# Performance work log

Hardware: AMD Instinct MI355X
Metric: run time of the kernel (lower is better)

The kernel has to match this reference:

```python
import jax, jax.numpy as jnp
import numpy as np

SCORE_THRESHOLD = 0.3
IOU_THRESHOLD = 0.5
TOP_K = 200
MAX_NMS_SIZE = 100
NEG = jnp.float32(-1e30)
NEG_HALF = jnp.float32(-1e29)


def _nms_per_class(scores, boxes):
    """Exact greedy NMS for one class. scores [N], boxes [N,4] (y1,x1,y2,x2).
    Returns (sel_scores [M], sel_boxes [M,4], valids [M]) with M=MAX_NMS_SIZE,
    zero-padded where fewer than M boxes survive (matches tf pad behavior)."""
    N = scores.shape[0]
    areas = jnp.prod(boxes[:, 2:] - boxes[:, :2], axis=-1)  # [N]
    arange_n = jnp.arange(N)
    # tf.image.non_max_suppression drops boxes with score < score_threshold
    masked0 = jnp.where(scores > SCORE_THRESHOLD, scores, NEG)

    def step(masked, _):
        idx = jnp.argmax(masked)
        s = masked[idx]
        valid = s > NEG_HALF
        box = boxes[idx]
        # IoU of selected box vs all boxes
        yx1 = jnp.maximum(box[:2], boxes[:, :2])
        yx2 = jnp.minimum(box[2:], boxes[:, 2:])
        inter = jnp.prod(jnp.maximum(yx2 - yx1, 0.0), axis=-1)
        union = jnp.prod(box[2:] - box[:2]) + areas - inter
        iou = jnp.where(union > 0, inter / union, 0.0)
        suppress = (iou > IOU_THRESHOLD) | (arange_n == idx)
        masked = jnp.where(valid & suppress, NEG, masked)
        return masked, (idx, valid, jnp.where(valid, s, 0.0))

    _, (idxs, valids, sel_scores) = jax.lax.scan(step, masked0, None, length=MAX_NMS_SIZE)
    sel_boxes = jnp.where(valids[:, None], boxes[idxs], 0.0)
    return sel_scores, sel_boxes, valids


def _per_sample(scores, boxes):
    """scores [N,C], boxes [N,4] -> (top_k_scores [K,2], top_k_boxes [K,4])."""
    cls_scores = scores[:, 1:].T  # [C-1, N]; class 0 (background) skipped
    sel_scores, sel_boxes, valids = jax.vmap(_nms_per_class, in_axes=(0, None))(cls_scores, boxes)
    ncls = cls_scores.shape[0]
    class_ids = jnp.where(valids, jnp.arange(1, ncls + 1, dtype=jnp.float32)[:, None], 0.0)
    flat_scores = jnp.stack([class_ids, sel_scores], axis=-1).reshape(-1, 2)  # [(C-1)*M, 2]
    flat_boxes = sel_boxes.reshape(-1, 4)
    n = flat_scores.shape[0]
    if TOP_K > n:  # static shapes -> Python-level pad branch
        flat_scores = jnp.pad(flat_scores, ((0, TOP_K - n), (0, 0)))
        flat_boxes = jnp.pad(flat_boxes, ((0, TOP_K - n), (0, 0)))
    _, top_idx = jax.lax.top_k(flat_scores[:, 1], TOP_K)
    return flat_scores[top_idx], flat_boxes[top_idx]


def setup_inputs() -> dict:
    key = jax.random.key(0)
    k1, k2, k3 = jax.random.split(key, 3)
    B, N, C = 16, 16384, 91
    scores_pred = jax.random.uniform(k1, (B, N, C), dtype=jnp.float32)
    tl = jax.random.uniform(k2, (B, N, 2), dtype=jnp.float32) * 0.8
    wh = jax.random.uniform(k3, (B, N, 2), dtype=jnp.float32) * 0.2 + 0.01
    boxes_pred = jnp.concatenate([tl, tl + wh], axis=-1)  # valid corner boxes
    return {"scores_pred": scores_pred, "boxes_pred": boxes_pred}


@jax.jit
def reference(scores_pred, boxes_pred):
    return jax.vmap(_per_sample)(scores_pred, boxes_pred)
```

## Files before the change

kernel.cpp:

```cpp
#include <hip/hip_runtime.h>

#define NTH 256
#define NBOX 16384
#define NCLSIN 91
#define NCLS 90
#define MAXSEL 100
#define TOPK 200
#define TSEL 256
#define CAP 1024
#define CANDL 512
#define CBCAP 256
#define BINS 1024
#define GRP 4
#define T0 0.989f
#define BOXPB 256
#define KSL 16
#define OVFC 64
#define CNTSTR 16

__device__ __forceinline__ unsigned fmap(float f) {
    unsigned u = __float_as_uint(f);
    return (u & 0x80000000u) ? ~u : (u | 0x80000000u);
}
__device__ __forceinline__ float funmap(unsigned u) {
    unsigned b = (u & 0x80000000u) ? (u ^ 0x80000000u) : ~u;
    return __uint_as_float(b);
}
__device__ __forceinline__ unsigned long long shfl_xor_u64(unsigned long long v, int mask) {
    unsigned lo = (unsigned)(v & 0xFFFFFFFFull);
    unsigned hi = (unsigned)(v >> 32);
    lo = __shfl_xor(lo, mask, 64);
    hi = __shfl_xor(hi, mask, 64);
    return ((unsigned long long)hi << 32) | (unsigned long long)lo;
}

__device__ __forceinline__ bool sup_test(float4 s, float sa, float4 c, float ca) {
    float y1 = fmaxf(s.x, c.x);
    float x1 = fmaxf(s.y, c.y);
    float y2 = fminf(s.z, c.z);
    float x2 = fminf(s.w, c.w);
    float dy = fmaxf(__fsub_rn(y2, y1), 0.f);
    float dx = fmaxf(__fsub_rn(x2, x1), 0.f);
    float inter = __fmul_rn(dy, dx);
    float uni = __fsub_rn(__fadd_rn(sa, ca), inter);
    if (!(uni > 0.f)) return false;
    float t = 0.5f * uni;
    if (inter <= t) return false;
    if (inter > __fmul_rn(t, 1.0000005f)) return true;
    return __fdiv_rn(inter, uni) > 0.5f;
}
__device__ __forceinline__ float box_area(float4 b) {
    return __fmul_rn(__fsub_rn(b.z, b.x), __fsub_rn(b.w, b.y));
}

__global__ __launch_bounds__(NTH) void zero_k(int4* __restrict__ p, int n4) {
    int i = blockIdx.x * NTH + threadIdx.x;
    if (i < n4) p[i] = make_int4(0, 0, 0, 0);
}

__device__ __forceinline__ void bin_select(unsigned* hist, unsigned* gbuf,
                                           int* sh_g, int* sh_b, unsigned* sh_pb,
                                           int tid, unsigned need) {
    unsigned gs = 0;
#pragma unroll
    for (int q = 0; q < GRP; ++q) gs += hist[tid * GRP + q];
    gbuf[tid] = gs;
    __syncthreads();
    for (int off = 1; off < NTH; off <<= 1) {
        unsigned add = (tid >= off) ? gbuf[tid - off] : 0u;
        __syncthreads();
        gbuf[tid] += add;
        __syncthreads();
    }
    if (tid == 0) *sh_g = NTH - 1;
    __syncthreads();
    if (gbuf[tid] >= need && (tid == 0 || gbuf[tid - 1] < need)) *sh_g = tid;
    __syncthreads();
    if (tid == 0) {
        int g = *sh_g;
        unsigned acc = (g > 0) ? gbuf[g - 1] : 0u;
        int bs = g * GRP + (GRP - 1);
        unsigned pb = acc;
#pragma unroll
        for (int q = 0; q < GRP; ++q) {
            acc += hist[g * GRP + q];
            if (acc >= need) { bs = g * GRP + q; pb = acc; break; }
            pb = acc;
        }
        *sh_b = bs; *sh_pb = pb;
    }
    __syncthreads();
}

__device__ __forceinline__ void sort_desc(unsigned long long* cand, int M, int tid) {
    int P = 1;
    while (P < M) P <<= 1;
    for (int i = M + tid; i < P; i += NTH) cand[i] = 0ull;
    __syncthreads();
    for (int kk = 2; kk <= P; kk <<= 1) {
        for (int jj = kk >> 1; jj > 0; jj >>= 1) {
            for (int i = tid; i < P; i += NTH) {
                int ixj = i ^ jj;
                if (ixj > i) {
                    unsigned long long a = cand[i], c = cand[ixj];
                    bool sw = ((i & kk) == 0) ? (a < c) : (a > c);
                    if (sw) { cand[i] = c; cand[ixj] = a; }
                }
            }
            __syncthreads();
        }
    }
}

__device__ __forceinline__ void emit_hit(unsigned long long pk, int b, int n0,
                                         int* cnt_s, unsigned long long* ent,
                                         unsigned* ovf_meta,
                                         unsigned long long* ovf_key,
                                         int* sh_ovf, int* cnt_g) {
    unsigned ee = (unsigned)pk;
    int row = (int)ee / NCLSIN;
    int c = (int)ee - row * NCLSIN;
    if (c == 0) return;
    unsigned i = (unsigned)(n0 + row);
    unsigned long long key = (pk & 0xFFFFFFFF00000000ull) | (0xFFFFFFFFu - i);
    int r = atomicAdd(&cnt_s[c], 1);
    if (r < KSL) {
        ent[c * KSL + r] = key;
    } else {
        int o = atomicAdd(sh_ovf, 1);
        if (o < OVFC) {
            ovf_meta[o] = ((unsigned)c << 16) | (unsigned)r;
            ovf_key[o] = key;
        } else {
            atomicAdd(&cnt_g[(b * NCLS + c - 1) * CNTSTR], CAP + 1);
        }
    }
}

__global__ __launch_bounds__(NTH) void filter_k(const float* __restrict__ in,
                                                unsigned long long* __restrict__ cand_g,
                                                int* __restrict__ cnt_g) {
    __shared__ int cnt_s[NCLSIN];
    __shared__ int base_s[NCLSIN];
    __shared__ unsigned long long ent[NCLSIN * KSL];
    __shared__ unsigned ovf_meta[OVFC];
    __shared__ unsigned long long ovf_key[OVFC];
    __shared__ int sh_ovf;

    const int tid = threadIdx.x;
    const int n0 = blockIdx.x * BOXPB;
    const int b = blockIdx.y;
    const int NF4 = BOXPB * NCLSIN / 4;

    for (int i = tid; i < NCLSIN; i += NTH) cnt_s[i] = 0;
    if (tid == 0) sh_ovf = 0;
    __syncthreads();

    unsigned long long q0 = 0, q1 = 0, q2 = 0, q3 = 0;
    int lc = 0;

    const float4* src = (const float4*)(in + ((size_t)b * NBOX + n0) * NCLSIN);
    for (int i = tid; i < NF4; i += 2 * NTH) {
        float4 v1 = src[i];
        int i2 = i + NTH;
        bool has2 = i2 < NF4;
        float4 v2 = make_float4(0.f, 0.f, 0.f, 0.f);
        if (has2) v2 = src[i2];
        float mx1 = fmaxf(fmaxf(v1.x, v1.y), fmaxf(v1.z, v1.w));
        float mx2 = fmaxf(fmaxf(v2.x, v2.y), fmaxf(v2.z, v2.w));
        if (fmaxf(mx1, mx2) > T0) {
#pragma unroll
            for (int h = 0; h < 2; ++h) {
                float4 v = h ? v2 : v1;
                float mx = h ? mx2 : mx1;
                int eb = (h ? i2 : i) * 4;
                if (mx > T0) {
                    const float sv[4] = {v.x, v.y, v.z, v.w};
#pragma unroll
                    for (int qq = 0; qq < 4; ++qq) {
                        float s = sv[qq];
                        if (s > T0) {
                            unsigned long long pk =
                                ((unsigned long long)fmap(s) << 32) |
                                (unsigned)(eb + qq);
                            if (lc == 0) q0 = pk;
                            else if (lc == 1) q1 = pk;
                            else if (lc == 2) q2 = pk;
                            else if (lc == 3) q3 = pk;
                            else emit_hit(pk, b, n0, cnt_s, ent, ovf_meta,
                                          ovf_key, &sh_ovf, cnt_g);
                            ++lc;
                        }
                    }
                }
            }
        }
    }
    if (lc > 0) emit_hit(q0, b, n0, cnt_s, ent, ovf_meta, ovf_key, &sh_ovf, cnt_g);
    if (lc > 1) emit_hit(q1, b, n0, cnt_s, ent, ovf_meta, ovf_key, &sh_ovf, cnt_g);
    if (lc > 2) emit_hit(q2, b, n0, cnt_s, ent, ovf_meta, ovf_key, &sh_ovf, cnt_g);
    if (lc > 3) emit_hit(q3, b, n0, cnt_s, ent, ovf_meta, ovf_key, &sh_ovf, cnt_g);
    __syncthreads();

    if (tid >= 1 && tid < NCLSIN) {
        int c = tid;
        int n = cnt_s[c];
        int base = 0;
        if (n > 0) {
            int bc = b * NCLS + c - 1;
            base = atomicAdd(&cnt_g[bc * CNTSTR], n);
            int lim = n < KSL ? n : KSL;
            for (int j = 0; j < lim; ++j) {
                int pos = base + j;
                if (pos < CAP) cand_g[(size_t)bc * CAP + pos] = ent[c * KSL + j];
            }
        }
        base_s[c] = base;
    }
    __syncthreads();

    int no = sh_ovf < OVFC ? sh_ovf : OVFC;
    for (int o = tid; o < no; o += NTH) {
        unsigned m = ovf_meta[o];
        int c = (int)(m >> 16);
        int r = (int)(m & 0xFFFFu);
        int bc = b * NCLS + c - 1;
        int pos = base_s[c] + r;
        if (pos < CAP) cand_g[(size_t)bc * CAP + pos] = ovf_key[o];
    }
}

__device__ __forceinline__ void walk_fast(
    const unsigned long long* cand, const float4* candbox, int M,
    float4& sel0, float4& sel1, float& sa0, float& sa1,
    float& ss0, float& ss1, int& nsel, int* sh_nsel, int tid) {
    if (tid < 64) {
        unsigned long long key_c = cand[0];
        float4 bx_c = candbox[0];
        for (int m = 0; m < M; ++m) {
            int mn = (m + 1 < M) ? m + 1 : m;
            unsigned long long key_n = cand[mn];
            float4 bx_n = candbox[mn];
            float ca = box_area(bx_c);
            bool sup = false;
            if (tid < nsel) sup = sup_test(sel0, sa0, bx_c, ca);
            if (tid + 64 < nsel) sup = sup || sup_test(sel1, sa1, bx_c, ca);
            if (!__any(sup)) {
                if (tid == nsel) { sel0 = bx_c; sa0 = ca; ss0 = funmap((unsigned)(key_c >> 32)); }
                if (tid == nsel - 64) { sel1 = bx_c; sa1 = ca; ss1 = funmap((unsigned)(key_c >> 32)); }
                nsel++;
                if (nsel >= MAXSEL) break;
            }
            key_c = key_n;
            bx_c = bx_n;
        }
        if (tid == 0) *sh_nsel = nsel;
    }
    __syncthreads();
    nsel = *sh_nsel;
    __syncthreads();
}

__device__ __forceinline__ void walk_slow(
    const unsigned long long* cand, int from, int to,
    const float4* __restrict__ bbase, const float4* candbox,
    float4& sel0, float4& sel1, float& sa0, float& sa1,
    float& ss0, float& ss1, int& nsel, int* sh_nsel, int tid) {
    if (tid < 64) {
        for (int m = from; m < to && nsel < MAXSEL; ++m) {
            unsigned long long key = cand[m];
            float4 bx = (m < CBCAP) ? candbox[m]
                                    : bbase[(int)(0xFFFFFFFFu - (unsigned)key)];
            float ca = box_area(bx);
            bool sup = false;
            if (tid < nsel) sup = sup_test(sel0, sa0, bx, ca);
            if (tid + 64 < nsel) sup = sup || sup_test(sel1, sa1, bx, ca);
            if (!__any(sup)) {
                if (tid == nsel) { sel0 = bx; sa0 = ca; ss0 = funmap((unsigned)(key >> 32)); }
                if (tid == nsel - 64) { sel1 = bx; sa1 = ca; ss1 = funmap((unsigned)(key >> 32)); }
                nsel++;
            }
        }
        if (tid == 0) *sh_nsel = nsel;
    }
    __syncthreads();
    nsel = *sh_nsel;
    __syncthreads();
}

__global__ __launch_bounds__(NTH) void nms_k(
    const unsigned long long* __restrict__ cand_g,
    const int* __restrict__ cnt_g,
    const float* __restrict__ scores_raw,
    const float4* __restrict__ boxes,
    float* __restrict__ ws_sc, float* __restrict__ ws_bx, int use_band) {
    __shared__ unsigned long long cand[CANDL];
    __shared__ float4 candbox[CBCAP];
    __shared__ unsigned gbuf[NTH];
    __shared__ unsigned sh_kmax, sh_pb;
    __shared__ int sh_E, sh_g, sh_b, sh_cnt, sh_nsel;
    unsigned* hist = (unsigned*)candbox;

    const int tid = threadIdx.x;
    const int c0 = blockIdx.x;
    const int b = blockIdx.y;
    const int bc = b * NCLS + c0;
    const float* sraw = scores_raw + (size_t)b * NBOX * NCLSIN + (c0 + 1);
    const float4* bbase = boxes + (size_t)b * NBOX;

    float4 sel0 = make_float4(0.f, 0.f, 0.f, 0.f);
    float4 sel1 = make_float4(0.f, 0.f, 0.f, 0.f);
    float sa0 = 0.f, sa1 = 0.f, ss0 = 0.f, ss1 = 0.f;
    int nsel = 0;
    unsigned long long lastk = ~0ull;

    if (use_band) {
        const int C = cnt_g[bc * CNTSTR];
        if (C > 0 && C <= CANDL) {
            if (C <= 256) {
                unsigned long long v =
                    (tid < C) ? cand_g[(size_t)bc * CAP + tid] : 0ull;
#pragma unroll
                for (int kk = 2; kk <= 256; kk <<= 1) {
#pragma unroll
                    for (int jj = kk >> 1; jj > 0; jj >>= 1) {
                        unsigned long long o;
                        if (jj >= 64) {
                            cand[tid] = v;
                            __syncthreads();
                            o = cand[tid ^ jj];
                            __syncthreads();
                        } else {
                            o = shfl_xor_u64(v, jj);
                        }
                        bool lower = (tid & jj) == 0;
                        bool desc = (tid & kk) == 0;
                        v = (lower == desc) ? (v > o ? v : o) : (v < o ? v : o);
                    }
                }
                cand[tid] = v;
                __syncthreads();
            } else {
                for (int i = tid; i < C; i += NTH)
                    cand[i] = cand_g[(size_t)bc * CAP + i];
                sort_desc(cand, C, tid);
            }
            const int PBX = C < CBCAP ? C : CBCAP;
            for (int i = tid; i < PBX; i += NTH)
                candbox[i] = bbase[(int)(0xFFFFFFFFu - (unsigned)cand[i])];
            __syncthreads();
            if (C <= CBCAP)
                walk_fast(cand, candbox, C, sel0, sel1, sa0, sa1,
                          ss0, ss1, nsel, &sh_nsel, tid);
            else
                walk_slow(cand, 0, C, bbase, candbox, sel0, sel1, sa0, sa1,
                          ss0, ss1, nsel, &sh_nsel, tid);
            lastk = cand[C - 1];
        }
    }

    while (nsel < MAXSEL) {
        unsigned km = 0, ce = 0;
        for (int i = tid; i < NBOX; i += NTH) {
            float s = sraw[(size_t)i * NCLSIN];
            unsigned k = (s > 0.3f) ? fmap(s) : 0u;
            if (k) {
                unsigned long long key =
                    ((unsigned long long)k << 32) | (0xFFFFFFFFu - (unsigned)i);
                if (key < lastk) { ce++; km = km > k ? km : k; }
            }
        }
#pragma unroll
        for (int off = 32; off > 0; off >>= 1) {
            unsigned o = (unsigned)__shfl_xor((int)km, off, 64);
            km = km > o ? km : o;
            ce += (unsigned)__shfl_xor((int)ce, off, 64);
        }
        if ((tid & 63) == 0) { gbuf[tid >> 6] = km; gbuf[8 + (tid >> 6)] = ce; }
        __syncthreads();
        if (tid == 0) {
            unsigned m2 = 0, c2 = 0;
            for (int w = 0; w < NTH / 64; ++w) {
                m2 = m2 > gbuf[w] ? m2 : gbuf[w];
                c2 += gbuf[8 + w];
            }
            sh_kmax = m2; sh_E = (int)c2;
        }
        __syncthreads();
        const int E = sh_E;
        const unsigned kmax = sh_kmax;
        if (E == 0) break;

        unsigned thr = 1u;
        if (E > TSEL) {
            for (int shift = 8;; shift += 4) {
                for (int i = tid; i < BINS; i += NTH) hist[i] = 0u;
                __syncthreads();
                for (int i = tid; i < NBOX; i += NTH) {
                    float s = sraw[(size_t)i * NCLSIN];
                    unsigned k = (s > 0.3f) ? fmap(s) : 0u;
                    if (k) {
                        unsigned long long key =
                            ((unsigned long long)k << 32) | (0xFFFFFFFFu - (unsigned)i);
                        if (key < lastk) {
                            unsigned bin = (kmax - k) >> shift;
                            if (bin < BINS - 1) atomicAdd(&hist[bin], 1u);
                        }
                    }
                }
                __syncthreads();
                bin_select(hist, gbuf, &sh_g, &sh_b, &sh_pb, tid, (unsigned)TSEL);
                if (sh_b < BINS - 1) {
                    long long t = (long long)kmax - ((long long)(sh_b + 1) << shift) + 1;
                    thr = (t < 1) ? 1u : (unsigned)t;
                    break;
                }
            }
        }

        if (tid == 0) sh_cnt = 0;
        __syncthreads();
        for (int i = tid; i < NBOX; i += NTH) {
            float s = sraw[(size_t)i * NCLSIN];
            unsigned k = (s > 0.3f) ? fmap(s) : 0u;
            if (k >= thr) {
                unsigned long long key =
                    ((unsigned long long)k << 32) | (0xFFFFFFFFu - (unsigned)i);
                if (key < lastk) {
                    int pos = atomicAdd(&sh_cnt, 1);
                    if (pos < CANDL) cand[pos] = key;
                }
            }
        }
        __syncthreads();
        const int M = sh_cnt < CANDL ? sh_cnt : CANDL;

        sort_desc(cand, M, tid);
        const int PBX = M < CBCAP ? M : CBCAP;
        for (int i = tid; i < PBX; i += NTH)
            candbox[i] = bbase[(int)(0xFFFFFFFFu - (unsigned)cand[i])];
        __syncthreads();
        walk_slow(cand, 0, M, bbase, candbox, sel0, sel1, sa0, sa1,
                  ss0, ss1, nsel, &sh_nsel, tid);
        if (nsel >= MAXSEL || E <= M) break;
        lastk = cand[M - 1];
        __syncthreads();
    }

    if (tid < 64) {
        float* scp = ws_sc + (size_t)bc * MAXSEL;
        float4* bxp = (float4*)(ws_bx + (size_t)bc * MAXSEL * 4);
        {
            bool v = tid < nsel;
            scp[tid] = v ? ss0 : 0.f;
            bxp[tid] = v ? sel0 : make_float4(0.f, 0.f, 0.f, 0.f);
        }
        int j1 = tid + 64;
        if (j1 < MAXSEL) {
            bool v = j1 < nsel;
            scp[j1] = v ? ss1 : 0.f;
            bxp[j1] = v ? sel1 : make_float4(0.f, 0.f, 0.f, 0.f);
        }
    }
}

__global__ __launch_bounds__(NTH) void topk_k(const float* __restrict__ ws_sc,
                                              const float* __restrict__ ws_bx,
                                              float* __restrict__ out_sc,
                                              float* __restrict__ out_bx) {
    __shared__ unsigned hist[BINS];
    __shared__ unsigned gbuf[NTH];
    __shared__ unsigned long long cand[CANDL];
    __shared__ unsigned sh_kmax, sh_pb;
    __shared__ int sh_E, sh_g, sh_b, sh_cnt;

    const int tid = threadIdx.x;
    const int b = blockIdx.x;
    const int NF = NCLS * MAXSEL;
    const float* sp = ws_sc + (size_t)b * NF;

    unsigned km = 0, ce = 0;
    for (int f = tid; f < NF; f += NTH) {
        unsigned k = __float_as_uint(sp[f]);
        if (k) { ce++; km = km > k ? km : k; }
    }
#pragma unroll
    for (int off = 32; off > 0; off >>= 1) {
        unsigned o = (unsigned)__shfl_xor((int)km, off, 64);
        km = km > o ? km : o;
        ce += (unsigned)__shfl_xor((int)ce, off, 64);
    }
    if ((tid & 63) == 0) { gbuf[tid >> 6] = km; gbuf[8 + (tid >> 6)] = ce; }
    __syncthreads();
    if (tid == 0) {
        unsigned m2 = 0, c2 = 0;
        for (int w = 0; w < NTH / 64; ++w) {
            m2 = m2 > gbuf[w] ? m2 : gbuf[w];
            c2 += gbuf[8 + w];
        }
        sh_kmax = m2; sh_E = (int)c2;
    }
    __syncthreads();
    const int E = sh_E;
    const unsigned kmax = sh_kmax;

    unsigned thr = 1u;
    if (E > TOPK) {
        for (int shift = 8;; shift += 4) {
            for (int i = tid; i < BINS; i += NTH) hist[i] = 0u;
            __syncthreads();
            for (int f = tid; f < NF; f += NTH) {
                unsigned k = __float_as_uint(sp[f]);
                if (k) {
                    unsigned bin = (kmax - k) >> shift;
                    if (bin < BINS - 1) atomicAdd(&hist[bin], 1u);
                }
            }
            __syncthreads();
            bin_select(hist, gbuf, &sh_g, &sh_b, &sh_pb, tid, (unsigned)TOPK);
            if (sh_b < BINS - 1) {
                long long t = (long long)kmax - ((long long)(sh_b + 1) << shift) + 1;
                thr = (t < 1) ? 1u : (unsigned)t;
                break;
            }
        }
    }

    if (tid == 0) sh_cnt = 0;
    __syncthreads();
    for (int f = tid; f < NF; f += NTH) {
        unsigned k = __float_as_uint(sp[f]);
        if (k >= thr) {
            int pos = atomicAdd(&sh_cnt, 1);
            if (pos < CANDL)
                cand[pos] = ((unsigned long long)k << 32) | (0xFFFFFFFFu - (unsigned)f);
        }
    }
    __syncthreads();
    int M = sh_cnt < CANDL ? sh_cnt : CANDL;

    if (M < TOPK) {
        int lim = M + TOPK;
        if (lim > NF) lim = NF;
        for (int f = tid; f < lim; f += NTH) {
            unsigned k = __float_as_uint(sp[f]);
            if (k == 0) {
                int pos = atomicAdd(&sh_cnt, 1);
                if (pos < CANDL)
                    cand[pos] = (unsigned long long)(0xFFFFFFFFu - (unsigned)f);
            }
        }
        __syncthreads();
        M = sh_cnt < CANDL ? sh_cnt : CANDL;
    }

    sort_desc(cand, M, tid);

    for (int k = tid; k < TOPK; k += NTH) {
        float cls = 0.f, s = 0.f;
        float4 bx = make_float4(0.f, 0.f, 0.f, 0.f);
        if (k < M) {
            unsigned long long key = cand[k];
            unsigned f = 0xFFFFFFFFu - (unsigned)key;
            s = __uint_as_float((unsigned)(key >> 32));
            cls = (s > 0.f) ? (float)(f / MAXSEL + 1) : 0.f;
            bx = *(const float4*)(ws_bx + ((size_t)b * NF + f) * 4);
        }
        out_sc[((size_t)b * TOPK + k) * 2 + 0] = cls;
        out_sc[((size_t)b * TOPK + k) * 2 + 1] = s;
        ((float4*)out_bx)[(size_t)b * TOPK + k] = bx;
    }
}

extern "C" void kernel_launch(void* const* d_in, const int* in_sizes, int n_in,
                              void* d_out, int out_size, void* d_ws, size_t ws_size,
                              hipStream_t stream) {
    const float* scores = (const float*)d_in[0];
    const float4* boxes = (const float4*)d_in[1];
    float* out = (float*)d_out;

    const int B = in_sizes[1] / (NBOX * 4);
    const int NBC = B * NCLS;

    size_t off_cand = ((size_t)NBC * CNTSTR * 4 + 15) & ~(size_t)15;
    size_t off_sc = off_cand + (size_t)NBC * CAP * 8;
    size_t off_bx = off_sc + (size_t)NBC * MAXSEL * 4;
    size_t need = off_bx + (size_t)NBC * MAXSEL * 16;

    char* ws = (char*)d_ws;
    bool use_band = ws_size >= need;

    int* cnt_g;
    unsigned long long* cand_g;
    float *ws_sc, *ws_bx;
    if (use_band) {
        cnt_g = (int*)ws;
        cand_g = (unsigned long long*)(ws + off_cand);
        ws_sc = (float*)(ws + off_sc);
        ws_bx = (float*)(ws + off_bx);
    } else {
        cnt_g = (int*)ws;
        cand_g = (unsigned long long*)ws;
        ws_sc = (float*)ws;
        ws_bx = ws_sc + (size_t)NBC * MAXSEL;
    }

    if (use_band) {
        int n4 = NBC * CNTSTR / 4;
        zero_k<<<(n4 + NTH - 1) / NTH, NTH, 0, stream>>>((int4*)cnt_g, n4);
        filter_k<<<dim3(NBOX / BOXPB, B), NTH, 0, stream>>>(scores, cand_g, cnt_g);
    }
    nms_k<<<dim3(NCLS, B), NTH, 0, stream>>>(cand_g, cnt_g, scores, boxes,
                                             ws_sc, ws_bx, use_band ? 1 : 0);
    topk_k<<<B, NTH, 0, stream>>>(ws_sc, ws_bx, out, out + (size_t)B * TOPK * 2);
}
```

Before: 114.0 us.

## Replace serial NMS walk with batched 64-wide suppression-matrix resolution

For small candidate sets (up to 256), the block precomputes a pairwise intra-batch suppression bitmask for each 64-candidate batch in parallel across all threads. Each batch is then resolved with one wave: the whole batch is tested against the already selected boxes, and intra-batch conflicts are settled with ballot and bitmask logic instead of one serial iteration per candidate. Selected boxes move from registers into shared memory, and candidate areas are precomputed. This trades the sequential per-candidate latency chain for extra pairwise IoU work and a loop over selected boxes per lane. The in-batch bitmask resolution looks like a single pass, so it may not exactly reproduce the greedy result.

```diff
diff --git a/kernel.cpp b/kernel.cpp
--- a/kernel.cpp
+++ b/kernel.cpp
@@ -230,54 +230,28 @@
     }
 }
 
-__device__ __forceinline__ void walk_fast(
-    const unsigned long long* cand, const float4* candbox, int M,
-    float4& sel0, float4& sel1, float& sa0, float& sa1,
-    float& ss0, float& ss1, int& nsel, int* sh_nsel, int tid) {
-    if (tid < 64) {
-        unsigned long long key_c = cand[0];
-        float4 bx_c = candbox[0];
-        for (int m = 0; m < M; ++m) {
-            int mn = (m + 1 < M) ? m + 1 : m;
-            unsigned long long key_n = cand[mn];
-            float4 bx_n = candbox[mn];
-            float ca = box_area(bx_c);
-            bool sup = false;
-            if (tid < nsel) sup = sup_test(sel0, sa0, bx_c, ca);
-            if (tid + 64 < nsel) sup = sup || sup_test(sel1, sa1, bx_c, ca);
-            if (!__any(sup)) {
-                if (tid == nsel) { sel0 = bx_c; sa0 = ca; ss0 = funmap((unsigned)(key_c >> 32)); }
-                if (tid == nsel - 64) { sel1 = bx_c; sa1 = ca; ss1 = funmap((unsigned)(key_c >> 32)); }
-                nsel++;
-                if (nsel >= MAXSEL) break;
-            }
-            key_c = key_n;
-            bx_c = bx_n;
-        }
-        if (tid == 0) *sh_nsel = nsel;
-    }
-    __syncthreads();
-    nsel = *sh_nsel;
-    __syncthreads();
-}
-
-__device__ __forceinline__ void walk_slow(
+__device__ __forceinline__ void serial_walk_lds(
     const unsigned long long* cand, int from, int to,
-    const float4* __restrict__ bbase, const float4* candbox,
-    float4& sel0, float4& sel1, float& sa0, float& sa1,
-    float& ss0, float& ss1, int& nsel, int* sh_nsel, int tid) {
+    const float4* __restrict__ bbase, const float4* candbox, const float* carea,
+    float4* selbox, float* selarea, float* selscore,
+    int& nsel, int* sh_nsel, int tid) {
     if (tid < 64) {
         for (int m = from; m < to && nsel < MAXSEL; ++m) {
             unsigned long long key = cand[m];
-            float4 bx = (m < CBCAP) ? candbox[m]
-                                    : bbase[(int)(0xFFFFFFFFu - (unsigned)key)];
-            float ca = box_area(bx);
+            float4 bx;
+            float ca;
+            if (m < CBCAP) { bx = candbox[m]; ca = carea[m]; }
+            else { bx = bbase[(int)(0xFFFFFFFFu - (unsigned)key)]; ca = box_area(bx); }
             bool sup = false;
-            if (tid < nsel) sup = sup_test(sel0, sa0, bx, ca);
-            if (tid + 64 < nsel) sup = sup || sup_test(sel1, sa1, bx, ca);
+            if (tid < nsel) sup = sup_test(selbox[tid], selarea[tid], bx, ca);
+            int l2 = tid + 64;
+            if (l2 < nsel) sup = sup || sup_test(selbox[l2], selarea[l2], bx, ca);
             if (!__any(sup)) {
-                if (tid == nsel) { sel0 = bx; sa0 = ca; ss0 = funmap((unsigned)(key >> 32)); }
-                if (tid == nsel - 64) { sel1 = bx; sa1 = ca; ss1 = funmap((unsigned)(key >> 32)); }
+                if (tid == 0) {
+                    selbox[nsel] = bx;
+                    selarea[nsel] = ca;
+                    selscore[nsel] = funmap((unsigned)(key >> 32));
+                }
                 nsel++;
             }
         }
@@ -296,6 +270,11 @@
     float* __restrict__ ws_sc, float* __restrict__ ws_bx, int use_band) {
     __shared__ unsigned long long cand[CANDL];
     __shared__ float4 candbox[CBCAP];
+    __shared__ float carea[CBCAP];
+    __shared__ float4 selbox[MAXSEL];
+    __shared__ float selarea[MAXSEL];
+    __shared__ float selscore[MAXSEL];
+    __shared__ unsigned M32[CBCAP * 2];
     __shared__ unsigned gbuf[NTH];
     __shared__ unsigned sh_kmax, sh_pb;
     __shared__ int sh_E, sh_g, sh_b, sh_cnt, sh_nsel;
@@ -308,9 +287,6 @@
     const float* sraw = scores_raw + (size_t)b * NBOX * NCLSIN + (c0 + 1);
     const float4* bbase = boxes + (size_t)b * NBOX;
 
-    float4 sel0 = make_float4(0.f, 0.f, 0.f, 0.f);
-    float4 sel1 = make_float4(0.f, 0.f, 0.f, 0.f);
-    float sa0 = 0.f, sa1 = 0.f, ss0 = 0.f, ss1 = 0.f;
     int nsel = 0;
     unsigned long long lastk = ~0ull;
 
@@ -340,21 +316,101 @@
                 }
                 cand[tid] = v;
                 __syncthreads();
+
+                if (tid < C) {
+                    float4 bx = bbase[(int)(0xFFFFFFFFu - (unsigned)cand[tid])];
+                    candbox[tid] = bx;
+                    carea[tid] = box_area(bx);
+                }
+                M32[tid] = 0;
+                M32[tid + NTH] = 0;
+                __syncthreads();
+
+                const int nbatch = (C + 63) >> 6;
+                for (int p = tid; p < nbatch * 2016; p += NTH) {
+                    int bt = p / 2016;
+                    int q = p - bt * 2016;
+                    int i = (int)((1.0f + sqrtf(1.0f + 8.0f * (float)q)) * 0.5f);
+                    while (i * (i - 1) / 2 > q) --i;
+                    while ((i + 1) * i / 2 <= q) ++i;
+                    int j = q - i * (i - 1) / 2;
+                    int gm = bt * 64 + i, gj = bt * 64 + j;
+                    if (gm < C) {
+                        if (sup_test(candbox[gj], carea[gj], candbox[gm], carea[gm]))
+                            atomicOr(&M32[gm * 2 + (j >> 5)], 1u << (j & 31));
+                    }
+                }
+                __syncthreads();
+
+                if (tid < 64) {
+                    for (int bt = 0; bt < nbatch && nsel < MAXSEL; ++bt) {
+                        int m = bt * 64 + tid;
+                        bool active = m < C;
+                        float4 bx = make_float4(0.f, 0.f, 0.f, 0.f);
+                        float ca = 0.f;
+                        unsigned long long key = 0ull;
+                        unsigned long long myM = 0ull;
+                        if (active) {
+                            key = cand[m];
+                            bx = candbox[m];
+                            ca = carea[m];
+                            myM = ((unsigned long long)M32[m * 2 + 1] << 32) |
+                                  M32[m * 2];
+                        }
+                        bool supV = !active;
+                        for (int j = 0; j < nsel; ++j) {
+                            if (active)
+                                supV = supV || sup_test(selbox[j], selarea[j], bx, ca);
+                        }
+                        unsigned long long selb = ~__ballot(supV);
+                        unsigned long long U = __ballot(myM != 0ull) & selb;
+                        while (U) {
+                            int mm = __builtin_ctzll(U);
+                            U &= U - 1ull;
+                            unsigned long long Mm =
+                                ((unsigned long long)M32[(bt * 64 + mm) * 2 + 1] << 32) |
+                                M32[(bt * 64 + mm) * 2];
+                            unsigned long long below =
+                                (mm == 0) ? 0ull : ((1ull << mm) - 1ull);
+                            if ((selb >> mm) & 1ull) {
+                                if (Mm & selb & below) selb &= ~(1ull << mm);
+                            }
+                        }
+                        int avail = MAXSEL - nsel;
+                        int pop = __builtin_popcountll(selb);
+                        while (pop > avail) {
+                            selb &= ~(1ull << (63 - __builtin_clzll(selb)));
+                            --pop;
+                        }
+                        if ((selb >> tid) & 1ull) {
+                            unsigned long long below =
+                                (tid == 0) ? 0ull : ((1ull << tid) - 1ull);
+                            int pos = nsel + __builtin_popcountll(selb & below);
+                            selbox[pos] = bx;
+                            selarea[pos] = ca;
+                            selscore[pos] = funmap((unsigned)(key >> 32));
+                        }
+                        nsel += pop;
+                    }
+                    if (tid == 0) sh_nsel = nsel;
+                }
+                __syncthreads();
+                nsel = sh_nsel;
+                __syncthreads();
             } else {
                 for (int i = tid; i < C; i += NTH)
                     cand[i] = cand_g[(size_t)bc * CAP + i];
                 sort_desc(cand, C, tid);
-            }
-            const int PBX = C < CBCAP ? C : CBCAP;
-            for (int i = tid; i < PBX; i += NTH)
-                candbox[i] = bbase[(int)(0xFFFFFFFFu - (unsigned)cand[i])];
-            __syncthreads();
-            if (C <= CBCAP)
-                walk_fast(cand, candbox, C, sel0, sel1, sa0, sa1,
-                          ss0, ss1, nsel, &sh_nsel, tid);
-            else
-                walk_slow(cand, 0, C, bbase, candbox, sel0, sel1, sa0, sa1,
-                          ss0, ss1, nsel, &sh_nsel, tid);
+                const int PBX = C < CBCAP ? C : CBCAP;
+                for (int i = tid; i < PBX; i += NTH) {
+                    float4 bx = bbase[(int)(0xFFFFFFFFu - (unsigned)cand[i])];
+                    candbox[i] = bx;
+                    carea[i] = box_area(bx);
+                }
+                __syncthreads();
+                serial_walk_lds(cand, 0, C, bbase, candbox, carea,
+                                selbox, selarea, selscore, nsel, &sh_nsel, tid);
+            }
             lastk = cand[C - 1];
         }
     }
@@ -437,30 +493,24 @@
 
         sort_desc(cand, M, tid);
         const int PBX = M < CBCAP ? M : CBCAP;
-        for (int i = tid; i < PBX; i += NTH)
-            candbox[i] = bbase[(int)(0xFFFFFFFFu - (unsigned)cand[i])];
-        __syncthreads();
-        walk_slow(cand, 0, M, bbase, candbox, sel0, sel1, sa0, sa1,
-                  ss0, ss1, nsel, &sh_nsel, tid);
+        for (int i = tid; i < PBX; i += NTH) {
+            float4 bx = bbase[(int)(0xFFFFFFFFu - (unsigned)cand[i])];
+            candbox[i] = bx;
+            carea[i] = box_area(bx);
+        }
+        __syncthreads();
+        serial_walk_lds(cand, 0, M, bbase, candbox, carea,
+                        selbox, selarea, selscore, nsel, &sh_nsel, tid);
         if (nsel >= MAXSEL || E <= M) break;
         lastk = cand[M - 1];
         __syncthreads();
     }
 
-    if (tid < 64) {
-        float* scp = ws_sc + (size_t)bc * MAXSEL;
-        float4* bxp = (float4*)(ws_bx + (size_t)bc * MAXSEL * 4);
-        {
-            bool v = tid < nsel;
-            scp[tid] = v ? ss0 : 0.f;
-            bxp[tid] = v ? sel0 : make_float4(0.f, 0.f, 0.f, 0.f);
-        }
-        int j1 = tid + 64;
-        if (j1 < MAXSEL) {
-            bool v = j1 < nsel;
-            scp[j1] = v ? ss1 : 0.f;
-            bxp[j1] = v ? sel1 : make_float4(0.f, 0.f, 0.f, 0.f);
-        }
+    if (tid < MAXSEL) {
+        bool v = tid < nsel;
+        ws_sc[(size_t)bc * MAXSEL + tid] = v ? selscore[tid] : 0.f;
+        ((float4*)ws_bx)[(size_t)bc * MAXSEL + tid] =
+            v ? selbox[tid] : make_float4(0.f, 0.f, 0.f, 0.f);
     }
 }
 
```

Measured after the change: 106.0 us. 7.1% less time.
